# Optimization experiments

Measured on AMD Instinct MI355X. Metric: run time of the kernel, lower is better.

The kernel has to match this reference:

```python
import jax, jax.numpy as jnp
import numpy as np

N_CUI, N_CODE, D = 100_000, 50_000, 128
F, L = 2, 2  # graph_num_filters, graph_num_layers
E_CC, E_KC, E_CK = 1_600_000, 800_000, 800_000


def setup_inputs() -> dict:
    key = jax.random.key(0)
    ks = jax.random.split(key, 11)
    x_cui = jax.random.normal(ks[0], (N_CUI, D), jnp.float32)
    x_code = jax.random.normal(ks[1], (N_CODE, D), jnp.float32)
    # edge_index tensors: row 0 = src, row 1 = dst
    ei_cc = jnp.stack([jax.random.randint(ks[2], (E_CC,), 0, N_CUI),
                       jax.random.randint(ks[3], (E_CC,), 0, N_CUI)])
    ei_kc = jnp.stack([jax.random.randint(ks[4], (E_KC,), 0, N_CODE),
                       jax.random.randint(ks[5], (E_KC,), 0, N_CUI)])
    ei_ck = jnp.stack([jax.random.randint(ks[6], (E_CK,), 0, N_CUI),
                       jax.random.randint(ks[7], (E_CK,), 0, N_CODE)])
    scale = 1.0 / np.sqrt(D)
    # [filter, layer, edge_type, D, D]; edge_type 0: cui->cui, 1: code->cui, 2: cui->code
    Wl = jax.random.normal(ks[8], (F, L, 3, D, D), jnp.float32) * scale
    Wr = jax.random.normal(ks[9], (F, L, 3, D, D), jnp.float32) * scale
    b = jax.random.normal(ks[10], (F, L, 3, D), jnp.float32) * 0.01
    return {"x_cui": x_cui, "x_code": x_code, "ei_cc": ei_cc, "ei_kc": ei_kc,
            "ei_ck": ei_ck, "Wl": Wl, "Wr": Wr, "b": b}


def _sage(x_src, x_dst, ei, Wl, Wr, b):
    """PyG SAGEConv(aggr='mean', normalize=False): lin_l(mean_msg) + lin_r(x_dst)."""
    n_dst = x_dst.shape[0]
    msg = x_src[ei[0]]  # [E, D] gather
    agg = jax.ops.segment_sum(msg, ei[1], num_segments=n_dst)  # [n_dst, D]
    cnt = jax.ops.segment_sum(jnp.ones((ei.shape[1],), msg.dtype), ei[1],
                              num_segments=n_dst)
    mean = agg / jnp.maximum(cnt, 1.0)[:, None]  # zero in-degree -> 0 (as PyG)
    return mean @ Wl.T + b + x_dst @ Wr.T


def reference(x_cui, x_code, ei_cc, ei_kc, ei_ck, Wl, Wr, b):
    outs_cui, outs_code = [], []
    for f in range(F):
        h_cui, h_code = x_cui, x_code
        for l in range(L):
            # HeteroConv aggr='sum': sum conv outputs per destination node type
            o_cui = (_sage(h_cui, h_cui, ei_cc, Wl[f, l, 0], Wr[f, l, 0], b[f, l, 0])
                     + _sage(h_code, h_cui, ei_kc, Wl[f, l, 1], Wr[f, l, 1], b[f, l, 1]))
            o_code = _sage(h_cui, h_code, ei_ck, Wl[f, l, 2], Wr[f, l, 2], b[f, l, 2])
            if l < L - 1:  # relu between layers only
                o_cui, o_code = jax.nn.relu(o_cui), jax.nn.relu(o_code)
            h_cui, h_code = o_cui, o_code
        outs_cui.append(h_cui)
        outs_code.append(h_code)
    # max over filter stacks
    out_cui = jnp.max(jnp.stack(outs_cui), axis=0)
    out_code = jnp.max(jnp.stack(outs_code), axis=0)
    return out_cui, out_code
```

## Files before the change

kernel.cpp:

```cpp
#include <hip/hip_runtime.h>

typedef unsigned short ushortT;
typedef __attribute__((ext_vector_type(8))) short short8v;
typedef __attribute__((ext_vector_type(4))) float float4v;

constexpr int D = 128;
constexpr int BKT_CAP = 8192;
constexpr int OVF_CAP = 1 << 20;

__device__ __forceinline__ void splitf(float v, short& h, short& l) {
    unsigned u = __float_as_uint(v);
    unsigned hb = u & 0xffff0000u;
    float r = v - __uint_as_float(hb);
    h = (short)(u >> 16);
    l = (short)(__float_as_uint(r) >> 16);
}
__device__ __forceinline__ unsigned packsplit(float v) {
    unsigned u = __float_as_uint(v);
    unsigned hb = u & 0xffff0000u;
    float r = v - __uint_as_float(hb);
    return hb | (__float_as_uint(r) >> 16);
}
__device__ __forceinline__ float unpackf(unsigned p) {
    return __uint_as_float(p & 0xffff0000u) + __uint_as_float(p << 16);
}

__global__ void bucket_count(const int* __restrict__ ecc, const int* __restrict__ ekc,
                             const int* __restrict__ eck, int Ecc, int Ekc, int Eck,
                             int ncui, int* __restrict__ cnt, int* __restrict__ bktCur,
                             unsigned* __restrict__ bkt, int* __restrict__ ovfCnt,
                             int* __restrict__ ovf) {
    int ET = Ecc + Ekc + Eck;
    for (int e = blockIdx.x * blockDim.x + threadIdx.x; e < ET;
         e += gridDim.x * blockDim.x) {
        int d, s;
        if (e < Ecc)            { s = ecc[e]; d = ecc[Ecc + e]; }
        else if (e < Ecc + Ekc) { int le = e - Ecc; s = ekc[le]; d = ncui + ekc[Ekc + le]; }
        else                    { int le = e - Ecc - Ekc; s = eck[le]; d = 2 * ncui + eck[Eck + le]; }
        atomicAdd(&cnt[d], 1);
        int b = d >> 8;
        int p = atomicAdd(&bktCur[b * 16], 1);
        if (p < BKT_CAP) {
            bkt[(size_t)b * BKT_CAP + p] = ((unsigned)(d & 255) << 24) | (unsigned)s;
        } else {
            int q = atomicAdd(ovfCnt, 1);
            if (q < OVF_CAP) { ovf[q * 2] = s; ovf[q * 2 + 1] = d; }
        }
    }
}

__global__ void bucket_place(const unsigned* __restrict__ bkt, const int* __restrict__ bktCur,
                             int* __restrict__ cur, int* __restrict__ csr) {
    int b = blockIdx.x;
    int n = bktCur[b * 16];
    if (n > BKT_CAP) n = BKT_CAP;
    int base = b << 8;
    for (int t = threadIdx.x; t < n; t += blockDim.x) {
        unsigned e = bkt[(size_t)b * BKT_CAP + t];
        int s = (int)(e & 0xFFFFFFu);
        int d = base + (int)(e >> 24);
        int p = atomicAdd(&cur[d], 1);
        csr[p] = s;
    }
}

__global__ void place_ovf(const int* __restrict__ ovfCnt, const int* __restrict__ ovf,
                          int* __restrict__ cur, int* __restrict__ csr) {
    int n = *ovfCnt;
    if (n > OVF_CAP) n = OVF_CAP;
    for (int i = blockIdx.x * blockDim.x + threadIdx.x; i < n;
         i += gridDim.x * blockDim.x) {
        int s = ovf[i * 2], d = ovf[i * 2 + 1];
        int p = atomicAdd(&cur[d], 1);
        csr[p] = s;
    }
}

__global__ __launch_bounds__(1024) void scan_s1(const int* __restrict__ cnt, int n4,
                                                int* __restrict__ blockSums) {
    __shared__ int red[1024];
    int t = threadIdx.x;
    int i = blockIdx.x * 1024 + t;
    int4 v = (i < n4) ? ((const int4*)cnt)[i] : make_int4(0, 0, 0, 0);
    red[t] = v.x + v.y + v.z + v.w;
    __syncthreads();
    for (int s = 512; s > 0; s >>= 1) {
        if (t < s) red[t] += red[t + s];
        __syncthreads();
    }
    if (t == 0) blockSums[blockIdx.x] = red[0];
}

__global__ __launch_bounds__(1024) void scan_s2(int* __restrict__ bs, int nb,
                                                int* __restrict__ offs, int NT) {
    __shared__ int s[1024];
    int t = threadIdx.x;
    int v = (t < nb) ? bs[t] : 0;
    s[t] = v;
    __syncthreads();
    for (int d = 1; d < 1024; d <<= 1) {
        int u = (t >= d) ? s[t - d] : 0;
        __syncthreads();
        s[t] += u;
        __syncthreads();
    }
    if (t < nb) bs[t] = s[t] - v;
    if (t == 0) offs[NT] = s[1023];
}

__global__ __launch_bounds__(1024) void scan_s3(const int* __restrict__ cnt, int n,
                                                const int* __restrict__ blockSums,
                                                int* __restrict__ offs, int* __restrict__ cur,
                                                float* __restrict__ inv) {
    __shared__ int sc[1024];
    int t = threadIdx.x;
    int n4 = n >> 2;
    int i4 = blockIdx.x * 1024 + t;
    int4 v = (i4 < n4) ? ((const int4*)cnt)[i4] : make_int4(0, 0, 0, 0);
    int s1 = v.x, s2 = s1 + v.y, s3 = s2 + v.z, s4 = s3 + v.w;
    sc[t] = s4;
    __syncthreads();
    for (int d = 1; d < 1024; d <<= 1) {
        int u = (t >= d) ? sc[t - d] : 0;
        __syncthreads();
        sc[t] += u;
        __syncthreads();
    }
    int base = sc[t] - s4 + blockSums[blockIdx.x];
    if (i4 < n4) {
        int4 o;
        o.x = base; o.y = base + s1; o.z = base + s2; o.w = base + s3;
        ((int4*)offs)[i4] = o;
        ((int4*)cur)[i4]  = o;
        float4 iv;
        iv.x = 1.f / fmaxf((float)v.x, 1.f);
        iv.y = 1.f / fmaxf((float)v.y, 1.f);
        iv.z = 1.f / fmaxf((float)v.z, 1.f);
        iv.w = 1.f / fmaxf((float)v.w, 1.f);
        ((float4*)inv)[i4] = iv;
    }
}

__global__ void prep_w(const float* __restrict__ Wl, const float* __restrict__ Wr,
                       const float* __restrict__ b, ushortT* __restrict__ Wp,
                       float* __restrict__ bcomb) {
    if (blockIdx.x == 160) {
        for (int t = threadIdx.x; t < 512; t += 256) {
            int fl = t >> 7, c = t & 127;
            bcomb[t] = b[(fl * 3 + 0) * D + c] + b[(fl * 3 + 1) * D + c];
        }
        return;
    }
    int id = blockIdx.x * 256 + threadIdx.x;
    int mat = id >> 11;
    int slot = id & 2047;
    int nt = slot >> 8, rem = slot & 255, ks = rem >> 6, lane = rem & 63;
    int row = nt * 16 + (lane & 15);
    int k0 = ks * 32 + ((lane >> 4) << 3);
    int fl = mat / 5, j = mat % 5;
    const float* s1;
    const float* s2 = nullptr;
    if (j < 2)       s1 = Wl + (size_t)(fl * 3 + j) * D * D;
    else if (j == 2) { s1 = Wr + (size_t)(fl * 3 + 0) * D * D;
                       s2 = Wr + (size_t)(fl * 3 + 1) * D * D; }
    else if (j == 3) s1 = Wl + (size_t)(fl * 3 + 2) * D * D;
    else             s1 = Wr + (size_t)(fl * 3 + 2) * D * D;

    unsigned hw[4], lw[4];
    #pragma unroll
    for (int q = 0; q < 4; ++q) {
        short h0, l0, h1, l1;
        float v0 = s1[row * D + k0 + 2 * q];
        float v1 = s1[row * D + k0 + 2 * q + 1];
        if (s2) { v0 += s2[row * D + k0 + 2 * q]; v1 += s2[row * D + k0 + 2 * q + 1]; }
        splitf(v0, h0, l0);
        splitf(v1, h1, l1);
        hw[q] = (unsigned short)h0 | ((unsigned)(unsigned short)h1 << 16);
        lw[q] = (unsigned short)l0 | ((unsigned)(unsigned short)l1 << 16);
    }
    ushortT* dh = Wp + (size_t)mat * 32768 + slot * 8;
    *(uint4*)dh           = make_uint4(hw[0], hw[1], hw[2], hw[3]);
    *(uint4*)(dh + 16384) = make_uint4(lw[0], lw[1], lw[2], lw[3]);
}

__global__ void agg_all(const float* __restrict__ src_cui_f, const float* __restrict__ src_code_f,
                        const unsigned* __restrict__ src_cui_p, const unsigned* __restrict__ src_code_p,
                        int packed, const int* __restrict__ csr, const int* __restrict__ offs,
                        const float* __restrict__ inv, int ncui, int ncode,
                        unsigned* __restrict__ outP) {
    int NT = 2 * ncui + ncode;
    int gw = (int)((blockIdx.x * (size_t)blockDim.x + threadIdx.x) >> 6);
    int lane = threadIdx.x & 63;
    if (gw >= NT) return;
    bool isCode = (gw >= ncui) && (gw < 2 * ncui);
    int st = offs[gw], en = offs[gw + 1];
    float ax[8], ay[8];
    #pragma unroll
    for (int j = 0; j < 8; ++j) { ax[j] = 0.f; ay[j] = 0.f; }
    int e = st;
    if (!packed) {
        const float* s = isCode ? src_code_f : src_cui_f;
        for (; e + 8 <= en; e += 8) {
            int idx[8];
            #pragma unroll
            for (int j = 0; j < 8; ++j) idx[j] = csr[e + j];
            #pragma unroll
            for (int j = 0; j < 8; ++j) {
                float2 q = ((const float2*)(s + (size_t)idx[j] * D))[lane];
                ax[j] += q.x; ay[j] += q.y;
            }
        }
        for (; e + 4 <= en; e += 4) {
            int idx[4];
            #pragma unroll
            for (int j = 0; j < 4; ++j) idx[j] = csr[e + j];
            #pragma unroll
            for (int j = 0; j < 4; ++j) {
                float2 q = ((const float2*)(s + (size_t)idx[j] * D))[lane];
                ax[j] += q.x; ay[j] += q.y;
            }
        }
        for (; e < en; ++e) {
            float2 q = ((const float2*)(s + (size_t)csr[e] * D))[lane];
            ax[0] += q.x; ay[0] += q.y;
        }
    } else {
        const unsigned* s = isCode ? src_code_p : src_cui_p;
        for (; e + 8 <= en; e += 8) {
            int idx[8];
            #pragma unroll
            for (int j = 0; j < 8; ++j) idx[j] = csr[e + j];
            #pragma unroll
            for (int j = 0; j < 8; ++j) {
                uint2 q = ((const uint2*)(s + (size_t)idx[j] * D))[lane];
                ax[j] += unpackf(q.x); ay[j] += unpackf(q.y);
            }
        }
        for (; e + 4 <= en; e += 4) {
            int idx[4];
            #pragma unroll
            for (int j = 0; j < 4; ++j) idx[j] = csr[e + j];
            #pragma unroll
            for (int j = 0; j < 4; ++j) {
                uint2 q = ((const uint2*)(s + (size_t)idx[j] * D))[lane];
                ax[j] += unpackf(q.x); ay[j] += unpackf(q.y);
            }
        }
        for (; e < en; ++e) {
            uint2 q = ((const uint2*)(s + (size_t)csr[e] * D))[lane];
            ax[0] += unpackf(q.x); ay[0] += unpackf(q.y);
        }
    }
    float sc = inv[gw];
    float r0 = (((ax[0] + ax[1]) + (ax[2] + ax[3])) + ((ax[4] + ax[5]) + (ax[6] + ax[7]))) * sc;
    float r1 = (((ay[0] + ay[1]) + (ay[2] + ay[3])) + ((ay[4] + ay[5]) + (ay[6] + ay[7]))) * sc;
    ((uint2*)(outP + (size_t)gw * D))[lane] = make_uint2(packsplit(r0), packsplit(r1));
}

__global__ __launch_bounds__(256, 2) void gemm_split(
    const unsigned* __restrict__ A0, const unsigned* __restrict__ A1,
    const unsigned* __restrict__ A2, const float* __restrict__ Alast_f32,
    const ushortT* __restrict__ W0, const ushortT* __restrict__ W1,
    const ushortT* __restrict__ W2, const float* __restrict__ bias,
    float* __restrict__ outF, unsigned* __restrict__ outP,
    int M, int nPairs, int mode) {
    __shared__ ushortT wlds[32768];

    int tid = threadIdx.x;
    int lane = tid & 63;
    int w = tid >> 6;
    int rowTile = blockIdx.x * 256 + w * 64;
    int rl = lane & 15;
    int kg = (lane >> 4) << 3;

    float4v acc[4][8];
    #pragma unroll
    for (int mt = 0; mt < 4; ++mt)
        #pragma unroll
        for (int nt = 0; nt < 8; ++nt)
            acc[mt][nt] = (float4v){0.f, 0.f, 0.f, 0.f};

    const unsigned* Aarr[3] = {A0, A1, A2};
    const ushortT* Warr[3] = {W0, W1, W2};

    for (int p = 0; p < nPairs; ++p) {
        __syncthreads();
        {
            const ushortT* Wsrc = Warr[p];
            #pragma unroll
            for (int i = 0; i < 16; ++i)
                *(int4*)&wlds[i * 2048 + tid * 8] = *(const int4*)&Wsrc[i * 2048 + tid * 8];
        }
        __syncthreads();
        bool f32A = (Alast_f32 != nullptr) && (p == nPairs - 1);
        const unsigned* A = Aarr[p];
        #pragma unroll
        for (int ks = 0; ks < 4; ++ks) {
            short8v ah[4], al[4];
            #pragma unroll
            for (int mt = 0; mt < 4; ++mt) {
                int row = rowTile + mt * 16 + rl;
                if (row < M) {
                    size_t boff = (size_t)row * D + ks * 32 + kg;
                    if (!f32A) {
                        uint4 q0 = *(const uint4*)(A + boff);
                        uint4 q1 = *(const uint4*)(A + boff + 4);
                        unsigned qa[8] = {q0.x, q0.y, q0.z, q0.w, q1.x, q1.y, q1.z, q1.w};
                        #pragma unroll
                        for (int jj = 0; jj < 8; ++jj) {
                            ah[mt][jj] = (short)(qa[jj] >> 16);
                            al[mt][jj] = (short)(qa[jj] & 0xffffu);
                        }
                    } else {
                        float4 f0 = *(const float4*)(Alast_f32 + boff);
                        float4 f1 = *(const float4*)(Alast_f32 + boff + 4);
                        float fa[8] = {f0.x, f0.y, f0.z, f0.w, f1.x, f1.y, f1.z, f1.w};
                        #pragma unroll
                        for (int jj = 0; jj < 8; ++jj) {
                            short hh, ll;
                            splitf(fa[jj], hh, ll);
                            ah[mt][jj] = hh;
                            al[mt][jj] = ll;
                        }
                    }
                } else {
                    #pragma unroll
                    for (int jj = 0; jj < 8; ++jj) { ah[mt][jj] = 0; al[mt][jj] = 0; }
                }
            }
            #pragma unroll
            for (int nt = 0; nt < 8; ++nt) {
                short8v bh = *(const short8v*)&wlds[nt * 2048 + ks * 512 + lane * 8];
                short8v bl = *(const short8v*)&wlds[16384 + nt * 2048 + ks * 512 + lane * 8];
                #pragma unroll
                for (int mt = 0; mt < 4; ++mt)
                    acc[mt][nt] = __builtin_amdgcn_mfma_f32_16x16x32_bf16(ah[mt], bh, acc[mt][nt], 0, 0, 0);
                #pragma unroll
                for (int mt = 0; mt < 4; ++mt)
                    acc[mt][nt] = __builtin_amdgcn_mfma_f32_16x16x32_bf16(ah[mt], bl, acc[mt][nt], 0, 0, 0);
                #pragma unroll
                for (int mt = 0; mt < 4; ++mt)
                    acc[mt][nt] = __builtin_amdgcn_mfma_f32_16x16x32_bf16(al[mt], bh, acc[mt][nt], 0, 0, 0);
            }
        }
    }

    #pragma unroll
    for (int nt = 0; nt < 8; ++nt) {
        int col = nt * 16 + rl;
        float bv = bias[col];
        #pragma unroll
        for (int mt = 0; mt < 4; ++mt) {
            int r0 = rowTile + mt * 16 + ((lane >> 4) << 2);
            float4v c = acc[mt][nt];
            #pragma unroll
            for (int r = 0; r < 4; ++r) {
                int row = r0 + r;
                if (row >= M) continue;
                float v = c[r] + bv;
                if (mode == 0) {
                    v = fmaxf(v, 0.f);
                    outP[(size_t)row * D + col] = packsplit(v);
                } else if (mode == 1) {
                    outF[(size_t)row * D + col] = v;
                } else {
                    float* pp = outF + (size_t)row * D + col;
                    *pp = fmaxf(*pp, v);
                }
            }
        }
    }
}

extern "C" void kernel_launch(void* const* d_in, const int* in_sizes, int n_in,
                              void* d_out, int out_size, void* d_ws, size_t ws_size,
                              hipStream_t stream) {
    const float* x_cui  = (const float*)d_in[0];
    const float* x_code = (const float*)d_in[1];
    const int*   ei_cc  = (const int*)d_in[2];
    const int*   ei_kc  = (const int*)d_in[3];
    const int*   ei_ck  = (const int*)d_in[4];
    const float* Wl     = (const float*)d_in[5];
    const float* Wr     = (const float*)d_in[6];
    const float* b      = (const float*)d_in[7];

    const int N_CUI  = in_sizes[0] / D;
    const int N_CODE = in_sizes[1] / D;
    const int E_CC   = in_sizes[2] / 2;
    const int E_KC   = in_sizes[3] / 2;
    const int E_CK   = in_sizes[4] / 2;
    const int NT = 2 * N_CUI + N_CODE;
    const int ET = E_CC + E_KC + E_CK;
    const int NB = (NT + 255) >> 8;

    char* ws = (char*)d_ws;
    size_t off = 0;
    auto alloc = [&](size_t bytes) -> char* {
        char* p = ws + off;
        off += (bytes + 255) & ~(size_t)255;
        return p;
    };

    int*      cntAll    = (int*)alloc((size_t)NT * 4);
    int*      bktCur    = (int*)alloc((size_t)NB * 16 * 4);
    int*      ovfCnt    = (int*)alloc(64);
    size_t cntBytes = off;

    int*      offsAll   = (int*)alloc(((size_t)NT + 4) * 4);
    int*      curAll    = (int*)alloc((size_t)NT * 4);
    float*    invAll    = (float*)alloc((size_t)NT * 4);
    int*      blockSums = (int*)alloc(1024 * 4);
    int*      csrAll    = (int*)alloc((size_t)ET * 4);
    ushortT*  Wp        = (ushortT*)alloc((size_t)20 * 32768 * 2);
    float*    bcomb     = (float*)alloc(512 * 4);
    unsigned* aggP      = (unsigned*)alloc((size_t)NT * D * 4);
    unsigned* hcuiP0    = (unsigned*)alloc((size_t)N_CUI * D * 4);
    unsigned* hcuiP1    = (unsigned*)alloc((size_t)N_CUI * D * 4);
    unsigned* hcodeP0   = (unsigned*)alloc((size_t)N_CODE * D * 4);
    unsigned* hcodeP1   = (unsigned*)alloc((size_t)N_CODE * D * 4);

    unsigned* bkt = aggP;
    int*      ovf = (int*)(aggP + (size_t)NB * BKT_CAP);

    float* out_cui  = (float*)d_out;
    float* out_code = (float*)d_out + (size_t)N_CUI * D;

    unsigned* hcP[2] = {hcuiP0, hcuiP1};
    unsigned* hkP[2] = {hcodeP0, hcodeP1};

    const unsigned* aggCC = aggP;
    const unsigned* aggKC = aggP + (size_t)N_CUI * D;
    const unsigned* aggCK = aggP + (size_t)2 * N_CUI * D;

    hipMemsetAsync(d_ws, 0, cntBytes, stream);
    bucket_count<<<2048, 256, 0, stream>>>(ei_cc, ei_kc, ei_ck, E_CC, E_KC, E_CK,
                                           N_CUI, cntAll, bktCur, bkt, ovfCnt, ovf);
    int n4 = NT >> 2;
    int nb = (n4 + 1023) / 1024;
    scan_s1<<<nb, 1024, 0, stream>>>(cntAll, n4, blockSums);
    scan_s2<<<1, 1024, 0, stream>>>(blockSums, nb, offsAll, NT);
    scan_s3<<<nb, 1024, 0, stream>>>(cntAll, NT, blockSums, offsAll, curAll, invAll);
    bucket_place<<<NB, 256, 0, stream>>>(bkt, bktCur, curAll, csrAll);
    place_ovf<<<64, 256, 0, stream>>>(ovfCnt, ovf, curAll, csrAll);
    prep_w<<<161, 256, 0, stream>>>(Wl, Wr, b, Wp, bcomb);

    int aggGrid = (NT + 3) / 4;
    int gCui = (N_CUI + 255) / 256;
    int gCode = (N_CODE + 255) / 256;
    auto WpM = [&](int m) { return (const ushortT*)(Wp + (size_t)m * 32768); };

    agg_all<<<aggGrid, 256, 0, stream>>>(x_cui, x_code, nullptr, nullptr, 0,
                                         csrAll, offsAll, invAll, N_CUI, N_CODE, aggP);
    for (int f = 0; f < 2; ++f) {
        int fl = f * 2;
        gemm_split<<<gCui, 256, 0, stream>>>(
            aggCC, aggKC, aggCC , x_cui,
            WpM(fl * 5 + 0), WpM(fl * 5 + 1), WpM(fl * 5 + 2),
            bcomb + fl * D, nullptr, hcP[f], N_CUI, 3, 0);
    }
    for (int f = 0; f < 2; ++f) {
        int fl = f * 2;
        gemm_split<<<gCode, 256, 0, stream>>>(
            aggCK, aggCK , aggCK , x_code,
            WpM(fl * 5 + 3), WpM(fl * 5 + 4), WpM(fl * 5 + 4),
            b + (size_t)(fl * 3 + 2) * D, nullptr, hkP[f], N_CODE, 2, 0);
    }

    for (int f = 0; f < 2; ++f) {
        int fl = f * 2 + 1;
        int mode = (f == 0) ? 1 : 2;
        agg_all<<<aggGrid, 256, 0, stream>>>(nullptr, nullptr, hcP[f], hkP[f], 1,
                                             csrAll, offsAll, invAll, N_CUI, N_CODE, aggP);
        gemm_split<<<gCui, 256, 0, stream>>>(
            aggCC, aggKC, hcP[f], nullptr,
            WpM(fl * 5 + 0), WpM(fl * 5 + 1), WpM(fl * 5 + 2),
            bcomb + fl * D, out_cui, nullptr, N_CUI, 3, mode);
        gemm_split<<<gCode, 256, 0, stream>>>(
            aggCK, hkP[f], hkP[f] , nullptr,
            WpM(fl * 5 + 3), WpM(fl * 5 + 4), WpM(fl * 5 + 4),
            b + (size_t)(fl * 3 + 2) * D, out_code, nullptr, N_CODE, 2, mode);
    }
}
```

Measured before the change: 1.882 ms.

## Replace global degree count and scan with per-bucket LDS counting sort

CSR construction drops the per-edge global atomicAdd on node degree counts and the three-kernel prefix scan. Each 256-node bucket is split into 8 sub-buckets keyed by block index, which spreads contention on the bucket cursors. A single-block scan computes bucket bases, and a per-bucket finalize kernel stages the edges in LDS, counts degrees locally, scans them and writes offsets, inverse degrees and CSR entries. Per-bucket capacity is tighter (8x1024), so more edges may go to the overflow path, and the finalize kernel uses 32KB of shared memory, which limits occupancy.

```diff
diff --git a/kernel.cpp b/kernel.cpp
--- a/kernel.cpp
+++ b/kernel.cpp
@@ -5,7 +5,7 @@
 typedef __attribute__((ext_vector_type(4))) float float4v;
 
 constexpr int D = 128;
-constexpr int BKT_CAP = 8192;
+constexpr int CAPC = 1024;
 constexpr int OVF_CAP = 1 << 20;
 
 __device__ __forceinline__ void splitf(float v, short& h, short& l) {
@@ -25,11 +25,12 @@
     return __uint_as_float(p & 0xffff0000u) + __uint_as_float(p << 16);
 }
 
-__global__ void bucket_count(const int* __restrict__ ecc, const int* __restrict__ ekc,
-                             const int* __restrict__ eck, int Ecc, int Ekc, int Eck,
-                             int ncui, int* __restrict__ cnt, int* __restrict__ bktCur,
-                             unsigned* __restrict__ bkt, int* __restrict__ ovfCnt,
-                             int* __restrict__ ovf) {
+__global__ void bucket_scatter(const int* __restrict__ ecc, const int* __restrict__ ekc,
+                               const int* __restrict__ eck, int Ecc, int Ekc, int Eck,
+                               int ncui, int* __restrict__ curC, unsigned* __restrict__ bktC,
+                               int* __restrict__ ovfCnt, int* __restrict__ ovf,
+                               int* __restrict__ bktOvf, int* __restrict__ cntExtra) {
+    int x = blockIdx.x & 7;
     int ET = Ecc + Ekc + Eck;
     for (int e = blockIdx.x * blockDim.x + threadIdx.x; e < ET;
          e += gridDim.x * blockDim.x) {
@@ -37,30 +38,108 @@
         if (e < Ecc)            { s = ecc[e]; d = ecc[Ecc + e]; }
         else if (e < Ecc + Ekc) { int le = e - Ecc; s = ekc[le]; d = ncui + ekc[Ekc + le]; }
         else                    { int le = e - Ecc - Ekc; s = eck[le]; d = 2 * ncui + eck[Eck + le]; }
-        atomicAdd(&cnt[d], 1);
         int b = d >> 8;
-        int p = atomicAdd(&bktCur[b * 16], 1);
-        if (p < BKT_CAP) {
-            bkt[(size_t)b * BKT_CAP + p] = ((unsigned)(d & 255) << 24) | (unsigned)s;
+        int p = atomicAdd(&curC[(b * 8 + x) * 16], 1);
+        if (p < CAPC) {
+            bktC[((size_t)b * 8 + x) * CAPC + p] = ((unsigned)(d & 255) << 24) | (unsigned)s;
         } else {
             int q = atomicAdd(ovfCnt, 1);
-            if (q < OVF_CAP) { ovf[q * 2] = s; ovf[q * 2 + 1] = d; }
-        }
-    }
-}
-
-__global__ void bucket_place(const unsigned* __restrict__ bkt, const int* __restrict__ bktCur,
-                             int* __restrict__ cur, int* __restrict__ csr) {
+            if (q < OVF_CAP) {
+                ovf[q * 2] = s; ovf[q * 2 + 1] = d;
+                atomicAdd(&bktOvf[b], 1);
+                atomicAdd(&cntExtra[d], 1);
+            }
+        }
+    }
+}
+
+__global__ __launch_bounds__(1024) void bucket_sums(const int* __restrict__ curC,
+                                                    const int* __restrict__ bktOvf,
+                                                    int NB, int NT, int* __restrict__ bktBase,
+                                                    int* __restrict__ offs) {
+    __shared__ int s[1024];
+    int t = threadIdx.x;
+    int tot = 0;
+    if (t < NB) {
+        #pragma unroll
+        for (int x = 0; x < 8; ++x) {
+            int c = curC[(t * 8 + x) * 16];
+            tot += (c > CAPC) ? CAPC : c;
+        }
+        tot += bktOvf[t];
+    }
+    s[t] = tot;
+    __syncthreads();
+    for (int d = 1; d < 1024; d <<= 1) {
+        int u = (t >= d) ? s[t - d] : 0;
+        __syncthreads();
+        s[t] += u;
+        __syncthreads();
+    }
+    if (t < NB) bktBase[t] = s[t] - tot;
+    if (t == 0) { bktBase[NB] = s[1023]; offs[NT] = s[1023]; }
+}
+
+__global__ __launch_bounds__(256) void bucket_finalize(
+    const unsigned* __restrict__ bktC, const int* __restrict__ curC,
+    const int* __restrict__ cntExtra, const int* __restrict__ bktBase, int NT,
+    int* __restrict__ offs, int* __restrict__ cur, float* __restrict__ inv,
+    int* __restrict__ csr) {
+    __shared__ unsigned stage[8 * CAPC];
+    __shared__ int lcnt[256], lofs[256], lcnt2[256], xbase[9];
     int b = blockIdx.x;
-    int n = bktCur[b * 16];
-    if (n > BKT_CAP) n = BKT_CAP;
-    int base = b << 8;
-    for (int t = threadIdx.x; t < n; t += blockDim.x) {
-        unsigned e = bkt[(size_t)b * BKT_CAP + t];
-        int s = (int)(e & 0xFFFFFFu);
-        int d = base + (int)(e >> 24);
-        int p = atomicAdd(&cur[d], 1);
-        csr[p] = s;
+    int t = threadIdx.x;
+    lcnt[t] = 0;
+    lcnt2[t] = 0;
+    if (t == 0) {
+        int acc = 0;
+        #pragma unroll
+        for (int x = 0; x < 8; ++x) {
+            xbase[x] = acc;
+            int c = curC[(b * 8 + x) * 16];
+            acc += (c > CAPC) ? CAPC : c;
+        }
+        xbase[8] = acc;
+    }
+    __syncthreads();
+    int ntot = xbase[8];
+    #pragma unroll
+    for (int x = 0; x < 8; ++x) {
+        int base = xbase[x], n = xbase[x + 1] - base;
+        const unsigned* src = bktC + ((size_t)b * 8 + x) * CAPC;
+        for (int i = t; i < n; i += 256) {
+            unsigned e = src[i];
+            stage[base + i] = e;
+            atomicAdd(&lcnt[e >> 24], 1);
+        }
+    }
+    __syncthreads();
+    int g = b * 256 + t;
+    int extra = (g < NT) ? cntExtra[g] : 0;
+    int tot = lcnt[t] + extra;
+    lofs[t] = tot;
+    __syncthreads();
+    for (int d = 1; d < 256; d <<= 1) {
+        int u = (t >= d) ? lofs[t - d] : 0;
+        __syncthreads();
+        lofs[t] += u;
+        __syncthreads();
+    }
+    int excl = lofs[t] - tot;
+    int base = bktBase[b];
+    if (g < NT) {
+        offs[g] = base + excl;
+        cur[g]  = base + excl + lcnt[t];
+        inv[g]  = 1.f / fmaxf((float)tot, 1.f);
+    }
+    __syncthreads();
+    lofs[t] = excl;
+    __syncthreads();
+    for (int i = t; i < ntot; i += 256) {
+        unsigned e = stage[i];
+        int ld = e >> 24;
+        int ord = atomicAdd(&lcnt2[ld], 1);
+        csr[base + lofs[ld] + ord] = (int)(e & 0xFFFFFFu);
     }
 }
 
@@ -73,71 +152,6 @@
         int s = ovf[i * 2], d = ovf[i * 2 + 1];
         int p = atomicAdd(&cur[d], 1);
         csr[p] = s;
-    }
-}
-
-__global__ __launch_bounds__(1024) void scan_s1(const int* __restrict__ cnt, int n4,
-                                                int* __restrict__ blockSums) {
-    __shared__ int red[1024];
-    int t = threadIdx.x;
-    int i = blockIdx.x * 1024 + t;
-    int4 v = (i < n4) ? ((const int4*)cnt)[i] : make_int4(0, 0, 0, 0);
-    red[t] = v.x + v.y + v.z + v.w;
-    __syncthreads();
-    for (int s = 512; s > 0; s >>= 1) {
-        if (t < s) red[t] += red[t + s];
-        __syncthreads();
-    }
-    if (t == 0) blockSums[blockIdx.x] = red[0];
-}
-
-__global__ __launch_bounds__(1024) void scan_s2(int* __restrict__ bs, int nb,
-                                                int* __restrict__ offs, int NT) {
-    __shared__ int s[1024];
-    int t = threadIdx.x;
-    int v = (t < nb) ? bs[t] : 0;
-    s[t] = v;
-    __syncthreads();
-    for (int d = 1; d < 1024; d <<= 1) {
-        int u = (t >= d) ? s[t - d] : 0;
-        __syncthreads();
-        s[t] += u;
-        __syncthreads();
-    }
-    if (t < nb) bs[t] = s[t] - v;
-    if (t == 0) offs[NT] = s[1023];
-}
-
-__global__ __launch_bounds__(1024) void scan_s3(const int* __restrict__ cnt, int n,
-                                                const int* __restrict__ blockSums,
-                                                int* __restrict__ offs, int* __restrict__ cur,
-                                                float* __restrict__ inv) {
-    __shared__ int sc[1024];
-    int t = threadIdx.x;
-    int n4 = n >> 2;
-    int i4 = blockIdx.x * 1024 + t;
-    int4 v = (i4 < n4) ? ((const int4*)cnt)[i4] : make_int4(0, 0, 0, 0);
-    int s1 = v.x, s2 = s1 + v.y, s3 = s2 + v.z, s4 = s3 + v.w;
-    sc[t] = s4;
-    __syncthreads();
-    for (int d = 1; d < 1024; d <<= 1) {
-        int u = (t >= d) ? sc[t - d] : 0;
-        __syncthreads();
-        sc[t] += u;
-        __syncthreads();
-    }
-    int base = sc[t] - s4 + blockSums[blockIdx.x];
-    if (i4 < n4) {
-        int4 o;
-        o.x = base; o.y = base + s1; o.z = base + s2; o.w = base + s3;
-        ((int4*)offs)[i4] = o;
-        ((int4*)cur)[i4]  = o;
-        float4 iv;
-        iv.x = 1.f / fmaxf((float)v.x, 1.f);
-        iv.y = 1.f / fmaxf((float)v.y, 1.f);
-        iv.z = 1.f / fmaxf((float)v.z, 1.f);
-        iv.w = 1.f / fmaxf((float)v.w, 1.f);
-        ((float4*)inv)[i4] = iv;
     }
 }
 
@@ -401,26 +415,27 @@
         return p;
     };
 
-    int*      cntAll    = (int*)alloc((size_t)NT * 4);
-    int*      bktCur    = (int*)alloc((size_t)NB * 16 * 4);
-    int*      ovfCnt    = (int*)alloc(64);
+    int*      curC     = (int*)alloc((size_t)NB * 8 * 16 * 4);
+    int*      ovfCnt   = (int*)alloc(64);
+    int*      bktOvf   = (int*)alloc((size_t)NB * 4);
+    int*      cntExtra = (int*)alloc((size_t)NT * 4);
     size_t cntBytes = off;
 
-    int*      offsAll   = (int*)alloc(((size_t)NT + 4) * 4);
-    int*      curAll    = (int*)alloc((size_t)NT * 4);
-    float*    invAll    = (float*)alloc((size_t)NT * 4);
-    int*      blockSums = (int*)alloc(1024 * 4);
-    int*      csrAll    = (int*)alloc((size_t)ET * 4);
-    ushortT*  Wp        = (ushortT*)alloc((size_t)20 * 32768 * 2);
-    float*    bcomb     = (float*)alloc(512 * 4);
-    unsigned* aggP      = (unsigned*)alloc((size_t)NT * D * 4);
-    unsigned* hcuiP0    = (unsigned*)alloc((size_t)N_CUI * D * 4);
-    unsigned* hcuiP1    = (unsigned*)alloc((size_t)N_CUI * D * 4);
-    unsigned* hcodeP0   = (unsigned*)alloc((size_t)N_CODE * D * 4);
-    unsigned* hcodeP1   = (unsigned*)alloc((size_t)N_CODE * D * 4);
-
-    unsigned* bkt = aggP;
-    int*      ovf = (int*)(aggP + (size_t)NB * BKT_CAP);
+    int*      offsAll  = (int*)alloc(((size_t)NT + 4) * 4);
+    int*      curAll   = (int*)alloc((size_t)NT * 4);
+    float*    invAll   = (float*)alloc((size_t)NT * 4);
+    int*      bktBase  = (int*)alloc(((size_t)NB + 1) * 4);
+    int*      csrAll   = (int*)alloc((size_t)ET * 4);
+    ushortT*  Wp       = (ushortT*)alloc((size_t)20 * 32768 * 2);
+    float*    bcomb    = (float*)alloc(512 * 4);
+    unsigned* aggP     = (unsigned*)alloc((size_t)NT * D * 4);
+    unsigned* hcuiP0   = (unsigned*)alloc((size_t)N_CUI * D * 4);
+    unsigned* hcuiP1   = (unsigned*)alloc((size_t)N_CUI * D * 4);
+    unsigned* hcodeP0  = (unsigned*)alloc((size_t)N_CODE * D * 4);
+    unsigned* hcodeP1  = (unsigned*)alloc((size_t)N_CODE * D * 4);
+
+    unsigned* bktC = aggP;
+    int*      ovf  = (int*)(aggP + (size_t)NB * 8 * CAPC);
 
     float* out_cui  = (float*)d_out;
     float* out_code = (float*)d_out + (size_t)N_CUI * D;
@@ -433,14 +448,11 @@
     const unsigned* aggCK = aggP + (size_t)2 * N_CUI * D;
 
     hipMemsetAsync(d_ws, 0, cntBytes, stream);
-    bucket_count<<<2048, 256, 0, stream>>>(ei_cc, ei_kc, ei_ck, E_CC, E_KC, E_CK,
-                                           N_CUI, cntAll, bktCur, bkt, ovfCnt, ovf);
-    int n4 = NT >> 2;
-    int nb = (n4 + 1023) / 1024;
-    scan_s1<<<nb, 1024, 0, stream>>>(cntAll, n4, blockSums);
-    scan_s2<<<1, 1024, 0, stream>>>(blockSums, nb, offsAll, NT);
-    scan_s3<<<nb, 1024, 0, stream>>>(cntAll, NT, blockSums, offsAll, curAll, invAll);
-    bucket_place<<<NB, 256, 0, stream>>>(bkt, bktCur, curAll, csrAll);
+    bucket_scatter<<<2048, 256, 0, stream>>>(ei_cc, ei_kc, ei_ck, E_CC, E_KC, E_CK,
+                                             N_CUI, curC, bktC, ovfCnt, ovf, bktOvf, cntExtra);
+    bucket_sums<<<1, 1024, 0, stream>>>(curC, bktOvf, NB, NT, bktBase, offsAll);
+    bucket_finalize<<<NB, 256, 0, stream>>>(bktC, curC, cntExtra, bktBase, NT,
+                                            offsAll, curAll, invAll, csrAll);
     place_ovf<<<64, 256, 0, stream>>>(ovfCnt, ovf, curAll, csrAll);
     prep_w<<<161, 256, 0, stream>>>(Wl, Wr, b, Wp, bcomb);
 
```

Result: faster. 1.642 ms (-12.8%).
